# Kernel optimization log

Measured on AMD Instinct MI355X. Metric: run time of the kernel, lower is better.

## Reference

```python
import jax, jax.numpy as jnp
import numpy as np

# ---- config (matches init_kwargs) ----
B, S, V = 8, 900, 11
H, NH, HD = 512, 8, 64          # hidden, heads, head_dim = H // NH
L = 2                            # num_layers
EXPANSION = 4.0
INNER = 1536                     # find_multiple(round(4.0 * 512 * 2/3), 256)
STEPS = 2                        # mcmc_num_steps
EPS = 1e-5                       # rms_norm_eps
THETA = 10000.0                  # rope_theta
ESCALE = float(np.sqrt(H))       # embed_scale = sqrt(hidden_size)
SCALE = 1.0 / float(np.sqrt(HD))


def rms_norm(x):
    return x * jax.lax.rsqrt(jnp.mean(x * x, axis=-1, keepdims=True) + EPS)


def rope_tables():
    inv_freq = 1.0 / (THETA ** (jnp.arange(0, HD, 2, dtype=jnp.float32) / HD))
    t = jnp.arange(S, dtype=jnp.float32)
    freqs = jnp.outer(t, inv_freq)                # (S, HD/2)
    emb = jnp.concatenate([freqs, freqs], axis=-1)  # (S, HD)
    return jnp.cos(emb), jnp.sin(emb)


def rotate_half(x):
    x1, x2 = jnp.split(x, 2, axis=-1)
    return jnp.concatenate([-x2, x1], axis=-1)


def apply_rope(q, k, cos, sin):
    cos = cos[None, :, None, :]  # (1,S,1,HD) broadcast over batch & heads
    sin = sin[None, :, None, :]
    return q * cos + rotate_half(q) * sin, k * cos + rotate_half(k) * sin


def block(h, qkv_w, o_w, gu_w, d_w, cos, sin):
    b, s, _ = h.shape
    qkv = (h @ qkv_w).reshape(b, s, 3 * NH, HD)
    q, k, v = qkv[:, :, :NH], qkv[:, :, NH:2 * NH], qkv[:, :, 2 * NH:]
    q, k = apply_rope(q, k, cos, sin)
    scores = jnp.einsum('bqhd,bkhd->bhqk', q, k) * SCALE
    attn = jax.nn.softmax(scores, axis=-1)
    out = jnp.einsum('bhqk,bkhd->bqhd', attn, v).reshape(b, s, NH * HD)
    h = rms_norm(h + out @ o_w)                   # post-norm residual
    gu = h @ gu_w
    gate, up = gu[..., :INNER], gu[..., INNER:]
    h = rms_norm(h + (jax.nn.silu(gate) * up) @ d_w)
    return h


def energy(logits, embed_w, energy_w, qkv_w, o_w, gu_w, d_w, input_emb, cos, sin):
    probs = jax.nn.softmax(logits, axis=-1)       # soft token distribution
    h = input_emb + ESCALE * (probs @ embed_w)    # soft embedding
    for i in range(L):
        h = block(h, qkv_w[i], o_w[i], gu_w[i], d_w[i], cos, sin)
    return jnp.sum(h @ energy_w)                  # scalar energy


def setup_inputs() -> dict:
    key = jax.random.key(0)
    ks = jax.random.split(key, 8)
    inputs = jax.random.randint(ks[0], (B, S), 0, V, dtype=jnp.int64)
    puzzle_identifiers = jax.random.randint(ks[1], (B,), 0, 1, dtype=jnp.int64)
    init_std = 1.0 / ESCALE
    embed_w = jax.random.normal(ks[2], (V, H), jnp.float32) * init_std
    energy_w = jax.random.normal(ks[3], (H, 1), jnp.float32) * 0.02
    qkv_w = jax.random.normal(ks[4], (L, H, 3 * NH * HD), jnp.float32) * 0.02
    o_w = jax.random.normal(ks[5], (L, NH * HD, H), jnp.float32) * 0.02
    gu_w = jax.random.normal(ks[6], (L, H, 2 * INNER), jnp.float32) * 0.02
    d_w = jax.random.normal(ks[7], (L, INNER, H), jnp.float32) * 0.02
    alpha = jnp.asarray(100.0, jnp.float32)       # mcmc_step_size
    return {"inputs": inputs, "puzzle_identifiers": puzzle_identifiers,
            "embed_w": embed_w, "energy_w": energy_w, "qkv_w": qkv_w,
            "o_w": o_w, "gu_w": gu_w, "d_w": d_w, "alpha": alpha}


def reference(inputs, puzzle_identifiers, embed_w, energy_w, qkv_w, o_w, gu_w, d_w, alpha):
    cos, sin = rope_tables()
    input_emb = ESCALE * embed_w[inputs]          # (B,S,H)
    a = jnp.maximum(alpha, 1e-4)                  # torch.clamp(alpha, min=1e-4)
    logits = jnp.zeros((inputs.shape[0], S, V), jnp.float32)
    egrad = jax.grad(energy)
    for _ in range(STEPS):                        # MCMC energy-descent loop
        g = egrad(logits, embed_w, energy_w, qkv_w, o_w, gu_w, d_w, input_emb, cos, sin)
        logits = logits - a * g
    return logits
```

## Files before the change

### kernel.cpp

```cpp
#include <hip/hip_runtime.h>
#include <math.h>

#define B_ 8
#define S_ 900
#define V_ 11
#define H_ 512
#define NH_ 8
#define HD_ 64
#define INNER_ 1536
#define STEPS_ 2
#define NTOK (B_*S_)
#define EPS_ 1e-5f
#define THETA_ 10000.0f
#define ESCALE_ 22.627416997969522f
#define SCALE_ 0.125f
#define PT_ 68

typedef __attribute__((ext_vector_type(8))) short bh8;
typedef __attribute__((ext_vector_type(4))) float f32x4;
typedef __attribute__((ext_vector_type(4))) unsigned short us4;

union bfu { bh8 v; unsigned short s[8]; us4 q[2]; };

__device__ inline unsigned short f2bf(float x) {
  unsigned u = __builtin_bit_cast(unsigned, x);
  return (unsigned short)((u + 0x7FFFu + ((u >> 16) & 1u)) >> 16);
}
__device__ inline float b2f(unsigned short s) {
  return __builtin_bit_cast(float, (unsigned)s << 16);
}

__device__ inline void gld16(const unsigned short* g, unsigned short* l) {
  __builtin_amdgcn_global_load_lds(
      (const __attribute__((address_space(1))) void*)(g),
      (__attribute__((address_space(3))) void*)(l), 16, 0, 0);
}

__device__ inline bh8 lds16(const unsigned short* p) {
  bfu u;
  u.q[0] = *(const us4*)p;
  u.q[1] = *(const us4*)(p + 4);
  return u.v;
}
__device__ inline void sts16(unsigned short* p, bfu u) {
  *(us4*)p = u.q[0];
  *(us4*)(p + 4) = u.q[1];
}

__device__ inline float wave_sum64(float x) {
#pragma unroll
  for (int off = 32; off > 0; off >>= 1) x += __shfl_xor(x, off, 64);
  return x;
}

__device__ inline float quad_sum(float x) {
  x += __shfl_xor(x, 1, 64);
  x += __shfl_xor(x, 2, 64);
  return x;
}


__global__ void k_zero(float* p, int n) {
  int i = blockIdx.x * blockDim.x + threadIdx.x;
  if (i < n) p[i] = 0.f;
}

__global__ void k_rope_tables(float* cs, float* sn) {
  int idx = blockIdx.x * blockDim.x + threadIdx.x;
  if (idx >= S_ * 32) return;
  int s = idx >> 5, i = idx & 31;
  float freq = powf(THETA_, -(float)i / 32.0f);
  float ang = (float)s * freq;
  cs[idx] = cosf(ang);
  sn[idx] = sinf(ang);
}

__global__ void k_softmax_logits(const float* __restrict__ logits, float* __restrict__ P) {
  int t = blockIdx.x * blockDim.x + threadIdx.x;
  if (t >= NTOK) return;
  float x[V_];
  float m = -1e30f;
#pragma unroll
  for (int v = 0; v < V_; ++v) { x[v] = logits[t * V_ + v]; m = fmaxf(m, x[v]); }
  float ssum = 0.f;
#pragma unroll
  for (int v = 0; v < V_; ++v) { x[v] = expf(x[v] - m); ssum += x[v]; }
  float inv = 1.f / ssum;
#pragma unroll
  for (int v = 0; v < V_; ++v) P[t * V_ + v] = x[v] * inv;
}

__global__ void k_h0(const float* __restrict__ P, const float* __restrict__ E,
                     const int* __restrict__ inp, float* __restrict__ h0,
                     unsigned short* __restrict__ h016) {
  int t = blockIdx.x;
  int tid = threadIdx.x;
  __shared__ float p[V_];
  __shared__ int iw;
  if (tid < V_) p[tid] = P[t * V_ + tid];
  if (tid == 0) iw = inp[t];
  __syncthreads();
  for (int h = tid; h < H_; h += blockDim.x) {
    float acc = E[iw * H_ + h];
#pragma unroll
    for (int v = 0; v < V_; ++v) acc += p[v] * E[v * H_ + h];
    float val = ESCALE_ * acc;
    h0[(size_t)t * H_ + h] = val;
    h016[(size_t)t * H_ + h] = f2bf(val);
  }
}

__global__ void k_gfill(const float* __restrict__ ew, float* __restrict__ G) {
  int idx = blockIdx.x * blockDim.x + threadIdx.x;
  if (idx < NTOK * H_) G[idx] = ew[idx & (H_ - 1)];
}

__global__ void k_cast8(const float* __restrict__ X, unsigned short* __restrict__ Y, int n8) {
  int i = blockIdx.x * blockDim.x + threadIdx.x;
  if (i >= n8) return;
  const float4* p = (const float4*)(X + (size_t)i * 8);
  float4 a = p[0], b = p[1];
  bfu o;
  o.s[0] = f2bf(a.x); o.s[1] = f2bf(a.y); o.s[2] = f2bf(a.z); o.s[3] = f2bf(a.w);
  o.s[4] = f2bf(b.x); o.s[5] = f2bf(b.y); o.s[6] = f2bf(b.z); o.s[7] = f2bf(b.w);
  *(bh8*)(Y + (size_t)i * 8) = o.v;
}


__global__ void k_wt(const float* __restrict__ W, unsigned short* __restrict__ WT, int K, int N) {
  __shared__ float t[32][33];
  int k0 = blockIdx.y * 32, n0 = blockIdx.x * 32;
  int tx = threadIdx.x, ty = threadIdx.y;
#pragma unroll
  for (int i = 0; i < 4; ++i)
    t[ty + 8 * i][tx] = W[(size_t)(k0 + ty + 8 * i) * N + n0 + tx];
  __syncthreads();
#pragma unroll
  for (int i = 0; i < 4; ++i)
    WT[(size_t)(n0 + ty + 8 * i) * K + k0 + tx] = f2bf(t[tx][ty + 8 * i]);
}


template <int TM, int SILU_A, int ADD, int CBF, int ROPE, int SILUBWD>
__global__ __launch_bounds__(256) void k_gemm(const unsigned short* __restrict__ A16,
                                              const unsigned short* __restrict__ Bt,
                                              const float* __restrict__ Dm,
                                              float* __restrict__ Cf,
                                              unsigned short* __restrict__ C16,
                                              unsigned short* __restrict__ GU,
                                              const float* __restrict__ Cs,
                                              const float* __restrict__ Sn,
                                              int M, int N, int K, int lda) {
  __shared__ unsigned short As[TM][32];
  __shared__ unsigned short Bs[128][32];
  constexpr int FR = TM / 32;
  int tid = threadIdx.x;
  int m0 = blockIdx.y * TM, n0 = blockIdx.x * 128;
  int wid = tid >> 6, lane = tid & 63;
  int wr = (wid >> 1) * (FR * 16), wc = (wid & 1) * 64;
  int lr = lane & 15, lg = lane >> 4;
  int srow = lane >> 2, sck = (lane & 3) * 8;
  f32x4 acc[FR][4] = {};
  for (int k0 = 0; k0 < K; k0 += 32) {
    __syncthreads();
#pragma unroll
    for (int half = 0; half < TM / 64; ++half) {
      if (SILU_A) {
        int row = (tid >> 2) + 64 * half;
        int ck = (tid & 3) * 8;
        int gr = m0 + row; gr = gr < M ? gr : M - 1;
        const unsigned short* src = &A16[(size_t)gr * lda + k0 + ck];
        bfu pa;
#pragma unroll
        for (int j = 0; j < 8; ++j) {
          float g = b2f(src[j]), u = b2f(src[INNER_ + j]);
          pa.s[j] = f2bf((g / (1.f + __expf(-g))) * u);
        }
        *(bh8*)&As[row][ck] = pa.v;
      } else {
        int gr = m0 + 64 * half + wid * 16 + srow; gr = gr < M ? gr : M - 1;
        gld16(&A16[(size_t)gr * lda + k0 + sck], &As[64 * half + wid * 16][0]);
      }
    }
#pragma unroll
    for (int i = 0; i < 2; ++i) {
      int bb = wid * 2 + i;
      gld16(&Bt[(size_t)(n0 + bb * 16 + srow) * K + k0 + sck], &Bs[bb * 16][0]);
    }
    __syncthreads();
    bh8 av[FR], bv[4];
#pragma unroll
    for (int fr = 0; fr < FR; ++fr) av[fr] = *(const bh8*)&As[wr + fr * 16 + lr][lg * 8];
#pragma unroll
    for (int fc = 0; fc < 4; ++fc) bv[fc] = *(const bh8*)&Bs[wc + fc * 16 + lr][lg * 8];
#pragma unroll
    for (int fr = 0; fr < FR; ++fr)
#pragma unroll
      for (int fc = 0; fc < 4; ++fc)
        acc[fr][fc] = __builtin_amdgcn_mfma_f32_16x16x32_bf16(av[fr], bv[fc], acc[fr][fc], 0, 0, 0);
  }
  bool rope_on = ROPE && (((n0 + wc) >> 6) < 16);
#pragma unroll
  for (int fr = 0; fr < FR; ++fr) {
    int r0 = m0 + wr + fr * 16 + lg * 4;
#pragma unroll
    for (int i = 0; i < 4; ++i) {
      int gr = r0 + i;
      if (gr >= M) continue;
      float c0 = 1.f, s0 = 0.f, c1 = 1.f, s1 = 0.f;
      if (ROPE) {
        if (rope_on) {
          int s = gr % S_;
          c0 = Cs[s * 32 + lr];      s0 = Sn[s * 32 + lr];
          c1 = Cs[s * 32 + 16 + lr]; s1 = Sn[s * 32 + 16 + lr];
        }
      }
#pragma unroll
      for (int fc = 0; fc < 4; ++fc) {
        int gc = n0 + wc + fc * 16 + lr;
        float out = acc[fr][fc][i];
        if (ROPE) {
          float part = acc[fr][fc ^ 2][i];
          float cc = (fc & 1) ? c1 : c0;
          float ss = (fc & 1) ? s1 : s0;
          out = (fc < 2) ? (out * cc - part * ss) : (out * cc + part * ss);
        }
        if (ADD) out += Dm[(size_t)gr * N + gc];
        if (SILUBWD) {
          size_t gb = (size_t)gr * (size_t)(2 * INNER_) + gc;
          float g = b2f(GU[gb]), u = b2f(GU[gb + INNER_]);
          float sig = 1.f / (1.f + __expf(-g));
          GU[gb] = f2bf(out * u * sig * (1.f + g * (1.f - sig)));
          GU[gb + INNER_] = f2bf(out * g * sig);
        } else if (CBF) {
          C16[(size_t)gr * N + gc] = f2bf(out);
        } else {
          Cf[(size_t)gr * N + gc] = out;
        }
      }
    }
  }
}


__global__ __launch_bounds__(256) void k_attn_fwd3(const unsigned short* __restrict__ QKV,
                                                   unsigned short* __restrict__ AO,
                                                   float* __restrict__ MB,
                                                   float* __restrict__ LB) {
  __shared__ unsigned short Ks[64][PT_];
  __shared__ unsigned short VT[64][PT_];
  __shared__ unsigned short Ps[4][16][PT_];
  int tid = threadIdx.x;
  int h = blockIdx.y, b = blockIdx.z;
  int w = tid >> 6, lane = tid & 63;
  int lr = lane & 15, lg = lane >> 4;
  int q0 = blockIdx.x * 64 + w * 16;

  bh8 qf[2];
  {
    int qr = q0 + lr; if (qr >= S_) qr = S_ - 1;
    const unsigned short* qp = &QKV[((size_t)(b * S_ + qr) * 24 + h) * 64 + lg * 8];
    qf[0] = *(const bh8*)qp;
    qf[1] = *(const bh8*)(qp + 32);
  }
  f32x4 accO[4] = {};
  float m[4], lsum[4];
#pragma unroll
  for (int i = 0; i < 4; ++i) { m[i] = -1e30f; lsum[i] = 0.f; }

  for (int kt = 0; kt < S_; kt += 64) {
    __syncthreads();
    {
      int r = tid >> 2, c0 = (tid & 3) * 16;
      int src = kt + r;
      size_t ts = (size_t)b * S_ + (src < S_ ? src : S_ - 1);
      const unsigned short* gp = &QKV[(ts * 24 + 8 + h) * 64 + c0];
      bfu p0, p1;
      p0.v = *(const bh8*)gp;
      p1.v = *(const bh8*)(gp + 8);
      sts16(&Ks[r][c0], p0);
      sts16(&Ks[r][c0 + 8], p1);
    }
    {
      int d0 = (tid & 15) * 4, k0r = (tid >> 4) * 4;
      us4 rv[4];
#pragma unroll
      for (int j = 0; j < 4; ++j) {
        int src = kt + k0r + j;
        size_t ts = (size_t)b * S_ + (src < S_ ? src : S_ - 1);
        rv[j] = *(const us4*)&QKV[(ts * 24 + 16 + h) * 64 + d0];
      }
#pragma unroll
      for (int dd = 0; dd < 4; ++dd) {
        us4 pk = {rv[0][dd], rv[1][dd], rv[2][dd], rv[3][dd]};
        *(us4*)&VT[d0 + dd][k0r] = pk;
      }
    }
    __syncthreads();
    f32x4 accS[4] = {};
#pragma unroll
    for (int ks = 0; ks < 2; ++ks)
#pragma unroll
      for (int fk = 0; fk < 4; ++fk)
        accS[fk] = __builtin_amdgcn_mfma_f32_16x16x32_bf16(qf[ks], lds16(&Ks[fk * 16 + lr][ks * 32 + lg * 8]), accS[fk], 0, 0, 0);
    float sc[4][4], pmax[4];
#pragma unroll
    for (int i = 0; i < 4; ++i) pmax[i] = -1e30f;
#pragma unroll
    for (int fk = 0; fk < 4; ++fk)
#pragma unroll
      for (int i = 0; i < 4; ++i) {
        float s = accS[fk][i] * SCALE_;
        if (kt + fk * 16 + lr >= S_) s = -1e30f;
        sc[fk][i] = s;
        pmax[i] = fmaxf(pmax[i], s);
      }
#pragma unroll
    for (int i = 0; i < 4; ++i) {
      float v = pmax[i];
      v = fmaxf(v, __shfl_xor(v, 1, 64));
      v = fmaxf(v, __shfl_xor(v, 2, 64));
      v = fmaxf(v, __shfl_xor(v, 4, 64));
      v = fmaxf(v, __shfl_xor(v, 8, 64));
      pmax[i] = v;
    }
    float psum[4];
#pragma unroll
    for (int i = 0; i < 4; ++i) {
      float mn = fmaxf(m[i], pmax[i]);
      float eo = __expf(m[i] - mn);
      m[i] = mn;
      lsum[i] *= eo;
#pragma unroll
      for (int fd = 0; fd < 4; ++fd) accO[fd][i] *= eo;
      psum[i] = 0.f;
    }
#pragma unroll
    for (int fk = 0; fk < 4; ++fk)
#pragma unroll
      for (int i = 0; i < 4; ++i) {
        float p = __expf(sc[fk][i] - m[i]);
        sc[fk][i] = p;
        psum[i] += p;
      }
#pragma unroll
    for (int i = 0; i < 4; ++i) {
      float v = psum[i];
      v += __shfl_xor(v, 1, 64);
      v += __shfl_xor(v, 2, 64);
      v += __shfl_xor(v, 4, 64);
      v += __shfl_xor(v, 8, 64);
      lsum[i] += v;
    }
#pragma unroll
    for (int fk = 0; fk < 4; ++fk)
#pragma unroll
      for (int i = 0; i < 4; ++i)
        Ps[w][lg * 4 + i][fk * 16 + lr] = f2bf(sc[fk][i]);
#pragma unroll
    for (int ks = 0; ks < 2; ++ks) {
      bh8 ap = lds16(&Ps[w][lr][ks * 32 + lg * 8]);
#pragma unroll
      for (int fd = 0; fd < 4; ++fd)
        accO[fd] = __builtin_amdgcn_mfma_f32_16x16x32_bf16(ap, lds16(&VT[fd * 16 + lr][ks * 32 + lg * 8]), accO[fd], 0, 0, 0);
    }
  }
#pragma unroll
  for (int i = 0; i < 4; ++i) {
    int q = q0 + lg * 4 + i;
    if (q < S_) {
      float linv = 1.f / lsum[i];
      size_t obase = (size_t)(b * S_ + q) * H_ + h * 64;
#pragma unroll
      for (int fd = 0; fd < 4; ++fd) AO[obase + fd * 16 + lr] = f2bf(accO[fd][i] * linv);
      if (lr == 0) {
        MB[((size_t)b * NH_ + h) * S_ + q] = m[i];
        LB[((size_t)b * NH_ + h) * S_ + q] = linv;
      }
    }
  }
}

__global__ __launch_bounds__(256) void k_delta(const unsigned short* __restrict__ O,
                                               const unsigned short* __restrict__ dO,
                                               float* __restrict__ DB) {
  int tid = threadIdx.x;
  int h = blockIdx.y, b = blockIdx.z;
  int r = blockIdx.x * 64 + (tid >> 2), part = tid & 3;
  if (r >= S_) return;
  size_t base = (size_t)(b * S_ + r) * H_ + h * 64 + part * 16;
  bfu o0, o1, d0, d1;
  o0.v = *(const bh8*)&O[base];  o1.v = *(const bh8*)&O[base + 8];
  d0.v = *(const bh8*)&dO[base]; d1.v = *(const bh8*)&dO[base + 8];
  float s = 0.f;
#pragma unroll
  for (int j = 0; j < 8; ++j)
    s += b2f(o0.s[j]) * b2f(d0.s[j]) + b2f(o1.s[j]) * b2f(d1.s[j]);
  s = quad_sum(s);
  if (part == 0) DB[((size_t)b * NH_ + h) * S_ + r] = s;
}

__global__ __launch_bounds__(256) void k_attn_bwd_dq3(const unsigned short* __restrict__ QKV,
                                                      const unsigned short* __restrict__ dO,
                                                      const float* __restrict__ MB,
                                                      const float* __restrict__ LB,
                                                      const float* __restrict__ DB,
                                                      const float* __restrict__ Cs,
                                                      const float* __restrict__ Sn,
                                                      unsigned short* __restrict__ dQKV) {
  __shared__ unsigned short Ks[64][PT_];
  __shared__ unsigned short Vs[64][PT_];
  __shared__ unsigned short KT[64][PT_];
  __shared__ unsigned short Ps[4][16][PT_];
  int tid = threadIdx.x;
  int h = blockIdx.y, b = blockIdx.z;
  int w = tid >> 6, lane = tid & 63;
  int lr = lane & 15, lg = lane >> 4;
  int q0 = blockIdx.x * 64 + w * 16;
  size_t sbase = ((size_t)b * NH_ + h) * S_;

  bh8 qf[2], dof[2];
  {
    int qr = q0 + lr; if (qr >= S_) qr = S_ - 1;
    const unsigned short* qp = &QKV[((size_t)(b * S_ + qr) * 24 + h) * 64 + lg * 8];
    const unsigned short* dp = &dO[(size_t)(b * S_ + qr) * H_ + h * 64 + lg * 8];
    qf[0] = *(const bh8*)qp;  qf[1] = *(const bh8*)(qp + 32);
    dof[0] = *(const bh8*)dp; dof[1] = *(const bh8*)(dp + 32);
  }
  float mrow[4], lrow[4], drow[4];
#pragma unroll
  for (int i = 0; i < 4; ++i) {
    int q = q0 + lg * 4 + i; if (q >= S_) q = S_ - 1;
    mrow[i] = MB[sbase + q];
    lrow[i] = LB[sbase + q];
    drow[i] = DB[sbase + q];
  }
  f32x4 accQ[4] = {};

  for (int kt = 0; kt < S_; kt += 64) {
    __syncthreads();
    {
      int r = tid >> 2, c0 = (tid & 3) * 16;
      int src = kt + r;
      bool vld = src < S_;
      size_t ts = (size_t)b * S_ + (vld ? src : S_ - 1);
      const unsigned short* kp = &QKV[(ts * 24 + 8 + h) * 64 + c0];
      bfu p0{}, p1{}, p2{}, p3{};
      if (vld) {
        p0.v = *(const bh8*)kp;
        p1.v = *(const bh8*)(kp + 8);
        p2.v = *(const bh8*)(kp + 512);
        p3.v = *(const bh8*)(kp + 520);
      }
      sts16(&Ks[r][c0], p0); sts16(&Ks[r][c0 + 8], p1);
      sts16(&Vs[r][c0], p2); sts16(&Vs[r][c0 + 8], p3);
    }
    {
      int d0 = (tid & 15) * 4, k0r = (tid >> 4) * 4;
      us4 rv[4];
#pragma unroll
      for (int j = 0; j < 4; ++j) {
        int src = kt + k0r + j;
        bool vld = src < S_;
        size_t ts = (size_t)b * S_ + (vld ? src : S_ - 1);
        us4 t = *(const us4*)&QKV[(ts * 24 + 8 + h) * 64 + d0];
        if (!vld) t = us4{0, 0, 0, 0};
        rv[j] = t;
      }
#pragma unroll
      for (int dd = 0; dd < 4; ++dd) {
        us4 pk = {rv[0][dd], rv[1][dd], rv[2][dd], rv[3][dd]};
        *(us4*)&KT[d0 + dd][k0r] = pk;
      }
    }
    __syncthreads();
    f32x4 aS[4] = {}, aD[4] = {};
#pragma unroll
    for (int ks = 0; ks < 2; ++ks)
#pragma unroll
      for (int fk = 0; fk < 4; ++fk) {
        aS[fk] = __builtin_amdgcn_mfma_f32_16x16x32_bf16(qf[ks], lds16(&Ks[fk * 16 + lr][ks * 32 + lg * 8]), aS[fk], 0, 0, 0);
        aD[fk] = __builtin_amdgcn_mfma_f32_16x16x32_bf16(dof[ks], lds16(&Vs[fk * 16 + lr][ks * 32 + lg * 8]), aD[fk], 0, 0, 0);
      }
#pragma unroll
    for (int fk = 0; fk < 4; ++fk)
#pragma unroll
      for (int i = 0; i < 4; ++i) {
        float p = __expf(aS[fk][i] * SCALE_ - mrow[i]) * lrow[i];
        float ds = p * (aD[fk][i] - drow[i]);
        Ps[w][lg * 4 + i][fk * 16 + lr] = f2bf(ds);
      }
#pragma unroll
    for (int ks = 0; ks < 2; ++ks) {
      bh8 ap = lds16(&Ps[w][lr][ks * 32 + lg * 8]);
#pragma unroll
      for (int fd = 0; fd < 4; ++fd)
        accQ[fd] = __builtin_amdgcn_mfma_f32_16x16x32_bf16(ap, lds16(&KT[fd * 16 + lr][ks * 32 + lg * 8]), accQ[fd], 0, 0, 0);
    }
  }
#pragma unroll
  for (int i = 0; i < 4; ++i) {
    int q = q0 + lg * 4 + i;
    if (q < S_) {
      size_t obase = ((size_t)(b * S_ + q) * 24 + h) * 64;
      float c0 = Cs[q * 32 + lr], s0 = Sn[q * 32 + lr];
      float c1 = Cs[q * 32 + 16 + lr], s1 = Sn[q * 32 + 16 + lr];
#pragma unroll
      for (int fd = 0; fd < 4; ++fd) {
        float x = SCALE_ * accQ[fd][i];
        float p = SCALE_ * accQ[fd ^ 2][i];
        float cc = (fd & 1) ? c1 : c0;
        float ss = (fd & 1) ? s1 : s0;
        float out = (fd < 2) ? (x * cc + p * ss) : (x * cc - p * ss);
        dQKV[obase + fd * 16 + lr] = f2bf(out);
      }
    }
  }
}

__global__ __launch_bounds__(256) void k_attn_bwd_kv3(const unsigned short* __restrict__ QKV,
                                                      const unsigned short* __restrict__ dO,
                                                      const float* __restrict__ MB,
                                                      const float* __restrict__ LB,
                                                      const float* __restrict__ DB,
                                                      const float* __restrict__ Cs,
                                                      const float* __restrict__ Sn,
                                                      unsigned short* __restrict__ dQKV) {
  __shared__ unsigned short Qs[64][PT_];
  __shared__ unsigned short dOs[64][PT_];
  __shared__ unsigned short QT[64][PT_];
  __shared__ unsigned short dOT[64][PT_];
  __shared__ unsigned short Ps[4][16][PT_];
  __shared__ float sM[64], sL[64], sD[64];
  int tid = threadIdx.x;
  int h = blockIdx.y, b = blockIdx.z;
  int w = tid >> 6, lane = tid & 63;
  int lr = lane & 15, lg = lane >> 4;
  int k0w = blockIdx.x * 64 + w * 16;
  size_t sbase = ((size_t)b * NH_ + h) * S_;

  bh8 kf[2], vf[2];
  {
    int kr = k0w + lr; if (kr >= S_) kr = S_ - 1;
    const unsigned short* kp = &QKV[((size_t)(b * S_ + kr) * 24 + 8 + h) * 64 + lg * 8];
    kf[0] = *(const bh8*)kp;        kf[1] = *(const bh8*)(kp + 32);
    vf[0] = *(const bh8*)(kp + 512); vf[1] = *(const bh8*)(kp + 544);
  }
  f32x4 accK[4] = {}, accV[4] = {};

  for (int qt = 0; qt < S_; qt += 64) {
    __syncthreads();
    {
      int r = tid >> 2, c0 = (tid & 3) * 16;
      int src = qt + r;
      bool vld = src < S_;
      size_t ts = (size_t)b * S_ + (vld ? src : S_ - 1);
      const unsigned short* qp = &QKV[(ts * 24 + h) * 64 + c0];
      const unsigned short* dp = &dO[ts * H_ + h * 64 + c0];
      bfu p0, p1, p2{}, p3{};
      p0.v = *(const bh8*)qp;
      p1.v = *(const bh8*)(qp + 8);
      if (vld) {
        p2.v = *(const bh8*)dp;
        p3.v = *(const bh8*)(dp + 8);
      }
      sts16(&Qs[r][c0], p0);  sts16(&Qs[r][c0 + 8], p1);
      sts16(&dOs[r][c0], p2); sts16(&dOs[r][c0 + 8], p3);
    }
    {
      int d0 = (tid & 15) * 4, q0r = (tid >> 4) * 4;
      us4 rq[4], rd[4];
#pragma unroll
      for (int j = 0; j < 4; ++j) {
        int src = qt + q0r + j;
        bool vld = src < S_;
        size_t ts = (size_t)b * S_ + (vld ? src : S_ - 1);
        rq[j] = *(const us4*)&QKV[(ts * 24 + h) * 64 + d0];
        us4 td = *(const us4*)&dO[ts * H_ + h * 64 + d0];
        if (!vld) td = us4{0, 0, 0, 0};
        rd[j] = td;
      }
#pragma unroll
      for (int dd = 0; dd < 4; ++dd) {
        us4 pq = {rq[0][dd], rq[1][dd], rq[2][dd], rq[3][dd]};
        us4 pd = {rd[0][dd], rd[1][dd], rd[2][dd], rd[3][dd]};
        *(us4*)&QT[d0 + dd][q0r] = pq;
        *(us4*)&dOT[d0 + dd][q0r] = pd;
      }
    }
    if (tid < 64) {
      int src = qt + tid;
      bool vld = src < S_;
      int sc = vld ? src : S_ - 1;
      sM[tid] = MB[sbase + sc];
      sL[tid] = LB[sbase + sc];
      sD[tid] = vld ? DB[sbase + sc] : 0.f;
    }
    __syncthreads();
    f32x4 aS[4] = {}, aD[4] = {};
#pragma unroll
    for (int ks = 0; ks < 2; ++ks)
#pragma unroll
      for (int fq = 0; fq < 4; ++fq) {
        aS[fq] = __builtin_amdgcn_mfma_f32_16x16x32_bf16(kf[ks], lds16(&Qs[fq * 16 + lr][ks * 32 + lg * 8]), aS[fq], 0, 0, 0);
        aD[fq] = __builtin_amdgcn_mfma_f32_16x16x32_bf16(vf[ks], lds16(&dOs[fq * 16 + lr][ks * 32 + lg * 8]), aD[fq], 0, 0, 0);
      }
    float pv[4][4];
#pragma unroll
    for (int fq = 0; fq < 4; ++fq) {
      float mq = sM[fq * 16 + lr], lq = sL[fq * 16 + lr];
#pragma unroll
      for (int i = 0; i < 4; ++i) {
        float p = __expf(aS[fq][i] * SCALE_ - mq) * lq;
        pv[fq][i] = p;
        Ps[w][lg * 4 + i][fq * 16 + lr] = f2bf(p);
      }
    }
#pragma unroll
    for (int qs = 0; qs < 2; ++qs) {
      bh8 ap = lds16(&Ps[w][lr][qs * 32 + lg * 8]);
#pragma unroll
      for (int fd = 0; fd < 4; ++fd)
        accV[fd] = __builtin_amdgcn_mfma_f32_16x16x32_bf16(ap, lds16(&dOT[fd * 16 + lr][qs * 32 + lg * 8]), accV[fd], 0, 0, 0);
    }
#pragma unroll
    for (int fq = 0; fq < 4; ++fq) {
      float dq = sD[fq * 16 + lr];
#pragma unroll
      for (int i = 0; i < 4; ++i)
        Ps[w][lg * 4 + i][fq * 16 + lr] = f2bf(pv[fq][i] * (aD[fq][i] - dq));
    }
#pragma unroll
    for (int qs = 0; qs < 2; ++qs) {
      bh8 ap = lds16(&Ps[w][lr][qs * 32 + lg * 8]);
#pragma unroll
      for (int fd = 0; fd < 4; ++fd)
        accK[fd] = __builtin_amdgcn_mfma_f32_16x16x32_bf16(ap, lds16(&QT[fd * 16 + lr][qs * 32 + lg * 8]), accK[fd], 0, 0, 0);
    }
  }
#pragma unroll
  for (int i = 0; i < 4; ++i) {
    int k = k0w + lg * 4 + i;
    if (k < S_) {
      size_t obase = ((size_t)(b * S_ + k) * 24 + 8 + h) * 64;
      float c0 = Cs[k * 32 + lr], s0 = Sn[k * 32 + lr];
      float c1 = Cs[k * 32 + 16 + lr], s1 = Sn[k * 32 + 16 + lr];
#pragma unroll
      for (int fd = 0; fd < 4; ++fd) {
        float x = SCALE_ * accK[fd][i];
        float p = SCALE_ * accK[fd ^ 2][i];
        float cc = (fd & 1) ? c1 : c0;
        float ss = (fd & 1) ? s1 : s0;
        float out = (fd < 2) ? (x * cc + p * ss) : (x * cc - p * ss);
        dQKV[obase + fd * 16 + lr] = f2bf(out);
        dQKV[obase + 512 + fd * 16 + lr] = f2bf(accV[fd][i]);
      }
    }
  }
}


__global__ __launch_bounds__(256) void k_rms_fwd(const float* __restrict__ X, float* __restrict__ Y,
                                                 unsigned short* __restrict__ Y16) {
  int t = blockIdx.x, tid = threadIdx.x;
  float x0 = X[(size_t)t * H_ + tid], x1 = X[(size_t)t * H_ + tid + 256];
  __shared__ float red[256];
  red[tid] = x0 * x0 + x1 * x1;
  __syncthreads();
  for (int s = 128; s > 0; s >>= 1) {
    if (tid < s) red[tid] += red[tid + s];
    __syncthreads();
  }
  float r = rsqrtf(red[0] / H_ + EPS_);
  float y0 = x0 * r, y1 = x1 * r;
  Y[(size_t)t * H_ + tid] = y0;
  Y[(size_t)t * H_ + tid + 256] = y1;
  Y16[(size_t)t * H_ + tid] = f2bf(y0);
  Y16[(size_t)t * H_ + tid + 256] = f2bf(y1);
}

__global__ __launch_bounds__(256) void k_rms_bwd(const float* __restrict__ X,
                                                 const float* __restrict__ GY,
                                                 float* __restrict__ GX,
                                                 unsigned short* __restrict__ GX16) {
  int t = blockIdx.x, tid = threadIdx.x;
  float x0 = X[(size_t)t * H_ + tid], x1 = X[(size_t)t * H_ + tid + 256];
  float g0 = GY[(size_t)t * H_ + tid], g1 = GY[(size_t)t * H_ + tid + 256];
  __shared__ float r1[256], r2[256];
  r1[tid] = x0 * x0 + x1 * x1;
  r2[tid] = x0 * g0 + x1 * g1;
  __syncthreads();
  for (int s = 128; s > 0; s >>= 1) {
    if (tid < s) { r1[tid] += r1[tid + s]; r2[tid] += r2[tid + s]; }
    __syncthreads();
  }
  float r = rsqrtf(r1[0] / H_ + EPS_);
  float coef = r * r * r * r2[0] / (float)H_;
  float o0 = r * g0 - coef * x0, o1 = r * g1 - coef * x1;
  GX[(size_t)t * H_ + tid] = o0;
  GX[(size_t)t * H_ + tid + 256] = o1;
  GX16[(size_t)t * H_ + tid] = f2bf(o0);
  GX16[(size_t)t * H_ + tid + 256] = f2bf(o1);
}


__global__ __launch_bounds__(64) void k_logits_update(const float* __restrict__ G,
                                                      const float* __restrict__ E,
                                                      const float* __restrict__ P,
                                                      const float* __restrict__ alpha,
                                                      float* __restrict__ logits) {
  int t = blockIdx.x, lane = threadIdx.x;
  float dp[V_];
#pragma unroll
  for (int v = 0; v < V_; ++v) dp[v] = 0.f;
  for (int hh = lane; hh < H_; hh += 64) {
    float gh = G[(size_t)t * H_ + hh];
#pragma unroll
    for (int v = 0; v < V_; ++v) dp[v] += gh * E[v * H_ + hh];
  }
#pragma unroll
  for (int v = 0; v < V_; ++v) dp[v] = wave_sum64(dp[v]) * ESCALE_;
  float dot = 0.f;
  float pv[V_];
#pragma unroll
  for (int v = 0; v < V_; ++v) {
    pv[v] = P[t * V_ + v];
    dot += pv[v] * dp[v];
  }
  float a = fmaxf(alpha[0], 1e-4f);
  if (lane < V_) logits[t * V_ + lane] -= a * pv[lane] * (dp[lane] - dot);
}


struct Ctx {
  unsigned short *Q16, *Q016, *dQ16, *GU16, *DO16, *AO16, *AO016, *X116, *UDX16, *U016;
  float *X1, *X2, *X20, *G, *UDX, *P, *MB, *LB, *DB, *MB0, *LB0, *CS, *SN;
  const unsigned short *WTqkv[2], *WTo[2], *WTgu[2], *WTd[2];
  const unsigned short *WSqkv[2], *WSo[2], *WSgu[2], *WSd[2];
  hipStream_t st;
};

static void block_forward(Ctx& c, int l, const float* hin, const unsigned short* hin16,
                          float* hout, unsigned short* qb, unsigned short* ao,
                          float* mb, float* lb, float* x2buf, unsigned short* u16buf) {
  k_gemm<128, 0, 0, 1, 1, 0><<<dim3(3 * H_ / 128, (NTOK + 127) / 128), 256, 0, c.st>>>(
      hin16, c.WTqkv[l], nullptr, nullptr, qb, nullptr, c.CS, c.SN, NTOK, 3 * H_, H_, H_);
  k_attn_fwd3<<<dim3((S_ + 63) / 64, NH_, B_), 256, 0, c.st>>>(qb, ao, mb, lb);
  k_gemm<64, 0, 1, 0, 0, 0><<<dim3(H_ / 128, (NTOK + 63) / 64), 256, 0, c.st>>>(
      ao, c.WTo[l], hin, c.X1, nullptr, nullptr, nullptr, nullptr, NTOK, H_, H_, H_);
  k_rms_fwd<<<NTOK, 256, 0, c.st>>>(c.X1, c.UDX, u16buf);
  k_gemm<128, 0, 0, 1, 0, 0><<<dim3(2 * INNER_ / 128, (NTOK + 127) / 128), 256, 0, c.st>>>(
      u16buf, c.WTgu[l], nullptr, nullptr, c.GU16, nullptr, nullptr, nullptr, NTOK, 2 * INNER_, H_, H_);
  k_gemm<64, 1, 1, 0, 0, 0><<<dim3(H_ / 128, (NTOK + 63) / 64), 256, 0, c.st>>>(
      c.GU16, c.WTd[l], c.UDX, x2buf, nullptr, nullptr, nullptr, nullptr, NTOK, H_, INNER_, 2 * INNER_);
  if (hout) k_rms_fwd<<<NTOK, 256, 0, c.st>>>(x2buf, hout, c.UDX16);
}

static void block_backward(Ctx& c, int l, const float* hin, const unsigned short* hin16,
                           unsigned short* qb, unsigned short* ao, float* mb, float* lb,
                           bool full) {
  const float* x2src;
  if (full) {
    block_forward(c, l, hin, hin16, nullptr, qb, ao, mb, lb, c.X2, c.UDX16);
    x2src = c.X2;
  } else {
    k_gemm<64, 0, 1, 0, 0, 0><<<dim3(H_ / 128, (NTOK + 63) / 64), 256, 0, c.st>>>(
        ao, c.WTo[l], hin, c.X1, nullptr, nullptr, nullptr, nullptr, NTOK, H_, H_, H_);
    k_gemm<128, 0, 0, 1, 0, 0><<<dim3(2 * INNER_ / 128, (NTOK + 127) / 128), 256, 0, c.st>>>(
        c.U016, c.WTgu[l], nullptr, nullptr, c.GU16, nullptr, nullptr, nullptr, NTOK, 2 * INNER_, H_, H_);
    x2src = c.X20;
  }
  k_rms_bwd<<<NTOK, 256, 0, c.st>>>(x2src, c.G, c.UDX, c.UDX16);
  k_gemm<128, 0, 0, 0, 0, 1><<<dim3(INNER_ / 128, (NTOK + 127) / 128), 256, 0, c.st>>>(
      c.UDX16, c.WSd[l], nullptr, nullptr, nullptr, c.GU16, nullptr, nullptr, NTOK, INNER_, H_, H_);
  k_gemm<64, 0, 1, 0, 0, 0><<<dim3(H_ / 128, (NTOK + 63) / 64), 256, 0, c.st>>>(
      c.GU16, c.WSgu[l], c.UDX, c.G, nullptr, nullptr, nullptr, nullptr, NTOK, H_, 2 * INNER_, 2 * INNER_);
  k_rms_bwd<<<NTOK, 256, 0, c.st>>>(c.X1, c.G, c.UDX, c.UDX16);
  k_gemm<64, 0, 0, 1, 0, 0><<<dim3(H_ / 128, (NTOK + 63) / 64), 256, 0, c.st>>>(
      c.UDX16, c.WSo[l], nullptr, nullptr, c.DO16, nullptr, nullptr, nullptr, NTOK, H_, H_, H_);
  dim3 agrid((S_ + 63) / 64, NH_, B_);
  k_delta<<<agrid, 256, 0, c.st>>>(ao, c.DO16, c.DB);
  k_attn_bwd_dq3<<<agrid, 256, 0, c.st>>>(qb, c.DO16, mb, lb, c.DB, c.CS, c.SN, c.dQ16);
  k_attn_bwd_kv3<<<agrid, 256, 0, c.st>>>(qb, c.DO16, mb, lb, c.DB, c.CS, c.SN, c.dQ16);
  k_gemm<64, 0, 1, 0, 0, 0><<<dim3(H_ / 128, (NTOK + 63) / 64), 256, 0, c.st>>>(
      c.dQ16, c.WSqkv[l], c.UDX, c.G, nullptr, nullptr, nullptr, nullptr, NTOK, H_, 3 * H_, 3 * H_);
}

extern "C" void kernel_launch(void* const* d_in, const int* in_sizes, int n_in,
                              void* d_out, int out_size, void* d_ws, size_t ws_size,
                              hipStream_t stream) {
  const int* inputs = (const int*)d_in[0];
  const float* E = (const float*)d_in[2];
  const float* ew = (const float*)d_in[3];
  const float* qkvw = (const float*)d_in[4];
  const float* ow = (const float*)d_in[5];
  const float* guw = (const float*)d_in[6];
  const float* dw = (const float*)d_in[7];
  const float* alpha = (const float*)d_in[8];
  float* logits = (float*)d_out;

  const size_t WT_FLOATS = 3407872;
  const size_t NEED =
      3 * ((size_t)NTOK * 3 * H_ / 2) +
      ((size_t)NTOK * INNER_) +
      5 * ((size_t)NTOK * H_) +
      6 * ((size_t)NTOK * H_ / 2) +
      ((size_t)NTOK * V_) +
      5 * ((size_t)B_ * NH_ * S_) +
      2 * ((size_t)S_ * 32) +
      2 * WT_FLOATS;
  if (ws_size < NEED * sizeof(float)) {
    k_zero<<<(NTOK * V_ + 255) / 256, 256, 0, stream>>>(logits, NTOK * V_);
    return;
  }

  float* f = (float*)d_ws;
  Ctx c;
  c.st = stream;
  c.Q16 = (unsigned short*)f;  f += (size_t)NTOK * 3 * H_ / 2;
  c.Q016 = (unsigned short*)f; f += (size_t)NTOK * 3 * H_ / 2;
  c.dQ16 = (unsigned short*)f; f += (size_t)NTOK * 3 * H_ / 2;
  c.GU16 = (unsigned short*)f; f += (size_t)NTOK * INNER_;
  c.X1 = f;   f += (size_t)NTOK * H_;
  c.X2 = f;   f += (size_t)NTOK * H_;
  c.X20 = f;  f += (size_t)NTOK * H_;
  c.G = f;    f += (size_t)NTOK * H_;
  c.UDX = f;  f += (size_t)NTOK * H_;
  c.AO16 = (unsigned short*)f;  f += (size_t)NTOK * H_ / 2;
  c.AO016 = (unsigned short*)f; f += (size_t)NTOK * H_ / 2;
  c.DO16 = (unsigned short*)f;  f += (size_t)NTOK * H_ / 2;
  c.X116 = (unsigned short*)f;  f += (size_t)NTOK * H_ / 2;
  c.UDX16 = (unsigned short*)f; f += (size_t)NTOK * H_ / 2;
  c.U016 = (unsigned short*)f;  f += (size_t)NTOK * H_ / 2;
  c.P = f;    f += (size_t)NTOK * V_;
  c.MB = f;   f += (size_t)B_ * NH_ * S_;
  c.LB = f;   f += (size_t)B_ * NH_ * S_;
  c.DB = f;   f += (size_t)B_ * NH_ * S_;
  c.MB0 = f;  f += (size_t)B_ * NH_ * S_;
  c.LB0 = f;  f += (size_t)B_ * NH_ * S_;
  c.CS = f;   f += (size_t)S_ * 32;
  c.SN = f;   f += (size_t)S_ * 32;
  unsigned short* wt = (unsigned short*)f;

  const size_t LQKV = (size_t)H_ * 3 * H_;
  const size_t LO = (size_t)H_ * H_;
  const size_t LGU = (size_t)H_ * 2 * INNER_;
  const size_t LD = (size_t)INNER_ * H_;

  for (int l = 0; l < 2; ++l) {
    c.WTqkv[l] = wt;
    k_wt<<<dim3(3 * H_ / 32, H_ / 32), dim3(32, 8), 0, stream>>>(qkvw + l * LQKV, wt, H_, 3 * H_);
    wt += LQKV;
    c.WTo[l] = wt;
    k_wt<<<dim3(H_ / 32, H_ / 32), dim3(32, 8), 0, stream>>>(ow + l * LO, wt, H_, H_);
    wt += LO;
    c.WTgu[l] = wt;
    k_wt<<<dim3(2 * INNER_ / 32, H_ / 32), dim3(32, 8), 0, stream>>>(guw + l * LGU, wt, H_, 2 * INNER_);
    wt += LGU;
    c.WTd[l] = wt;
    k_wt<<<dim3(H_ / 32, INNER_ / 32), dim3(32, 8), 0, stream>>>(dw + l * LD, wt, INNER_, H_);
    wt += LD;
  }
  {
    unsigned short* ws = wt;
    k_cast8<<<(int)((2 * LQKV / 8 + 255) / 256), 256, 0, stream>>>(qkvw, ws, (int)(2 * LQKV / 8));
    c.WSqkv[0] = ws; c.WSqkv[1] = ws + LQKV; ws += 2 * LQKV;
    k_cast8<<<(int)((2 * LO / 8 + 255) / 256), 256, 0, stream>>>(ow, ws, (int)(2 * LO / 8));
    c.WSo[0] = ws; c.WSo[1] = ws + LO; ws += 2 * LO;
    k_cast8<<<(int)((2 * LGU / 8 + 255) / 256), 256, 0, stream>>>(guw, ws, (int)(2 * LGU / 8));
    c.WSgu[0] = ws; c.WSgu[1] = ws + LGU; ws += 2 * LGU;
    k_cast8<<<(int)((2 * LD / 8 + 255) / 256), 256, 0, stream>>>(dw, ws, (int)(2 * LD / 8));
    c.WSd[0] = ws; c.WSd[1] = ws + LD;
  }

  k_zero<<<(NTOK * V_ + 255) / 256, 256, 0, stream>>>(logits, NTOK * V_);
  k_rope_tables<<<(S_ * 32 + 255) / 256, 256, 0, stream>>>(c.CS, c.SN);

  for (int step = 0; step < STEPS_; ++step) {
    k_softmax_logits<<<(NTOK + 255) / 256, 256, 0, stream>>>(logits, c.P);
    k_h0<<<NTOK, 256, 0, stream>>>(c.P, E, inputs, c.X1, c.X116);
    block_forward(c, 0, c.X1, c.X116, c.UDX, c.Q016, c.AO016, c.MB0, c.LB0, c.X20, c.U016);
    k_gfill<<<(NTOK * H_ + 255) / 256, 256, 0, stream>>>(ew, c.G);
    block_backward(c, 1, c.UDX, c.UDX16, c.Q16, c.AO16, c.MB, c.LB, true);
    k_h0<<<NTOK, 256, 0, stream>>>(c.P, E, inputs, c.X1, c.X116);
    block_backward(c, 0, c.X1, c.X116, c.Q016, c.AO016, c.MB0, c.LB0, false);
    k_logits_update<<<NTOK, 64, 0, stream>>>(c.G, E, c.P, alpha, logits);
  }
}
```

Measured before the change: 2.430 ms.

## Prefetch next K/V/Q/dO tiles into registers in attention kernels

In the forward attention kernel and both backward kernels (dQ and dK/dV), the global loads for the next 64-row tile are now issued into registers right after the current tile is written to shared memory. This lets global-memory latency overlap the MFMA and softmax work of the current iteration, at the cost of more live registers per thread. The shared-memory row padding also changes from 68 to 70 elements to alter the bank mapping. A 140-byte row stride breaks 16-byte and 8-byte alignment of the vector LDS reads and writes, which risks split or slower LDS accesses.

```diff
diff --git a/kernel.cpp b/kernel.cpp
--- a/kernel.cpp
+++ b/kernel.cpp
@@ -14,7 +14,7 @@
 #define THETA_ 10000.0f
 #define ESCALE_ 22.627416997969522f
 #define SCALE_ 0.125f
-#define PT_ 68
+#define PT_ 70
 
 typedef __attribute__((ext_vector_type(8))) short bh8;
 typedef __attribute__((ext_vector_type(4))) float f32x4;
@@ -255,6 +255,8 @@
   int w = tid >> 6, lane = tid & 63;
   int lr = lane & 15, lg = lane >> 4;
   int q0 = blockIdx.x * 64 + w * 16;
+  int sr = tid >> 2, sc0 = (tid & 3) * 16;
+  int vd0 = (tid & 15) * 4, vk0 = (tid >> 4) * 4;
 
   bh8 qf[2];
   {
@@ -268,32 +270,42 @@
 #pragma unroll
   for (int i = 0; i < 4; ++i) { m[i] = -1e30f; lsum[i] = 0.f; }
 
+  bfu kA, kB;
+  us4 vR[4];
+  {
+    int src = sr;
+    size_t ts = (size_t)b * S_ + (src < S_ ? src : S_ - 1);
+    const unsigned short* gp = &QKV[(ts * 24 + 8 + h) * 64 + sc0];
+    kA.v = *(const bh8*)gp;
+    kB.v = *(const bh8*)(gp + 8);
+#pragma unroll
+    for (int j = 0; j < 4; ++j) {
+      int s2 = vk0 + j;
+      size_t t2 = (size_t)b * S_ + (s2 < S_ ? s2 : S_ - 1);
+      vR[j] = *(const us4*)&QKV[(t2 * 24 + 16 + h) * 64 + vd0];
+    }
+  }
+
   for (int kt = 0; kt < S_; kt += 64) {
     __syncthreads();
-    {
-      int r = tid >> 2, c0 = (tid & 3) * 16;
-      int src = kt + r;
+    sts16(&Ks[sr][sc0], kA);
+    sts16(&Ks[sr][sc0 + 8], kB);
+#pragma unroll
+    for (int dd = 0; dd < 4; ++dd) {
+      us4 pk = {vR[0][dd], vR[1][dd], vR[2][dd], vR[3][dd]};
+      *(us4*)&VT[vd0 + dd][vk0] = pk;
+    }
+    if (kt + 64 < S_) {
+      int src = kt + 64 + sr;
       size_t ts = (size_t)b * S_ + (src < S_ ? src : S_ - 1);
-      const unsigned short* gp = &QKV[(ts * 24 + 8 + h) * 64 + c0];
-      bfu p0, p1;
-      p0.v = *(const bh8*)gp;
-      p1.v = *(const bh8*)(gp + 8);
-      sts16(&Ks[r][c0], p0);
-      sts16(&Ks[r][c0 + 8], p1);
-    }
-    {
-      int d0 = (tid & 15) * 4, k0r = (tid >> 4) * 4;
-      us4 rv[4];
+      const unsigned short* gp = &QKV[(ts * 24 + 8 + h) * 64 + sc0];
+      kA.v = *(const bh8*)gp;
+      kB.v = *(const bh8*)(gp + 8);
 #pragma unroll
       for (int j = 0; j < 4; ++j) {
-        int src = kt + k0r + j;
-        size_t ts = (size_t)b * S_ + (src < S_ ? src : S_ - 1);
-        rv[j] = *(const us4*)&QKV[(ts * 24 + 16 + h) * 64 + d0];
-      }
-#pragma unroll
-      for (int dd = 0; dd < 4; ++dd) {
-        us4 pk = {rv[0][dd], rv[1][dd], rv[2][dd], rv[3][dd]};
-        *(us4*)&VT[d0 + dd][k0r] = pk;
+        int s2 = kt + 64 + vk0 + j;
+        size_t t2 = (size_t)b * S_ + (s2 < S_ ? s2 : S_ - 1);
+        vR[j] = *(const us4*)&QKV[(t2 * 24 + 16 + h) * 64 + vd0];
       }
     }
     __syncthreads();
@@ -418,6 +430,8 @@
   int lr = lane & 15, lg = lane >> 4;
   int q0 = blockIdx.x * 64 + w * 16;
   size_t sbase = ((size_t)b * NH_ + h) * S_;
+  int sr = tid >> 2, sc0 = (tid & 3) * 16;
+  int vd0 = (tid & 15) * 4, vk0 = (tid >> 4) * 4;
 
   bh8 qf[2], dof[2];
   {
@@ -437,40 +451,59 @@
   }
   f32x4 accQ[4] = {};
 
+  bfu pA{}, pB{}, pC{}, pD{};
+  us4 rv[4];
+  {
+    int src = sr;
+    bool vld = src < S_;
+    size_t ts = (size_t)b * S_ + (vld ? src : S_ - 1);
+    const unsigned short* kp = &QKV[(ts * 24 + 8 + h) * 64 + sc0];
+    if (vld) {
+      pA.v = *(const bh8*)kp;
+      pB.v = *(const bh8*)(kp + 8);
+      pC.v = *(const bh8*)(kp + 512);
+      pD.v = *(const bh8*)(kp + 520);
+    }
+#pragma unroll
+    for (int j = 0; j < 4; ++j) {
+      int s2 = vk0 + j;
+      bool v2 = s2 < S_;
+      size_t t2 = (size_t)b * S_ + (v2 ? s2 : S_ - 1);
+      us4 t = *(const us4*)&QKV[(t2 * 24 + 8 + h) * 64 + vd0];
+      if (!v2) t = us4{0, 0, 0, 0};
+      rv[j] = t;
+    }
+  }
+
   for (int kt = 0; kt < S_; kt += 64) {
     __syncthreads();
-    {
-      int r = tid >> 2, c0 = (tid & 3) * 16;
-      int src = kt + r;
+    sts16(&Ks[sr][sc0], pA); sts16(&Ks[sr][sc0 + 8], pB);
+    sts16(&Vs[sr][sc0], pC); sts16(&Vs[sr][sc0 + 8], pD);
+#pragma unroll
+    for (int dd = 0; dd < 4; ++dd) {
+      us4 pk = {rv[0][dd], rv[1][dd], rv[2][dd], rv[3][dd]};
+      *(us4*)&KT[vd0 + dd][vk0] = pk;
+    }
+    if (kt + 64 < S_) {
+      int src = kt + 64 + sr;
       bool vld = src < S_;
       size_t ts = (size_t)b * S_ + (vld ? src : S_ - 1);
-      const unsigned short* kp = &QKV[(ts * 24 + 8 + h) * 64 + c0];
-      bfu p0{}, p1{}, p2{}, p3{};
+      const unsigned short* kp = &QKV[(ts * 24 + 8 + h) * 64 + sc0];
+      pA = bfu{}; pB = bfu{}; pC = bfu{}; pD = bfu{};
       if (vld) {
-        p0.v = *(const bh8*)kp;
-        p1.v = *(const bh8*)(kp + 8);
-        p2.v = *(const bh8*)(kp + 512);
-        p3.v = *(const bh8*)(kp + 520);
-      }
-      sts16(&Ks[r][c0], p0); sts16(&Ks[r][c0 + 8], p1);
-      sts16(&Vs[r][c0], p2); sts16(&Vs[r][c0 + 8], p3);
-    }
-    {
-      int d0 = (tid & 15) * 4, k0r = (tid >> 4) * 4;
-      us4 rv[4];
+        pA.v = *(const bh8*)kp;
+        pB.v = *(const bh8*)(kp + 8);
+        pC.v = *(const bh8*)(kp + 512);
+        pD.v = *(const bh8*)(kp + 520);
+      }
 #pragma unroll
       for (int j = 0; j < 4; ++j) {
-        int src = kt + k0r + j;
-        bool vld = src < S_;
-        size_t ts = (size_t)b * S_ + (vld ? src : S_ - 1);
-        us4 t = *(const us4*)&QKV[(ts * 24 + 8 + h) * 64 + d0];
-        if (!vld) t = us4{0, 0, 0, 0};
+        int s2 = kt + 64 + vk0 + j;
+        bool v2 = s2 < S_;
+        size_t t2 = (size_t)b * S_ + (v2 ? s2 : S_ - 1);
+        us4 t = *(const us4*)&QKV[(t2 * 24 + 8 + h) * 64 + vd0];
+        if (!v2) t = us4{0, 0, 0, 0};
         rv[j] = t;
-      }
-#pragma unroll
-      for (int dd = 0; dd < 4; ++dd) {
-        us4 pk = {rv[0][dd], rv[1][dd], rv[2][dd], rv[3][dd]};
-        *(us4*)&KT[d0 + dd][k0r] = pk;
       }
     }
     __syncthreads();
@@ -538,6 +571,8 @@
   int lr = lane & 15, lg = lane >> 4;
   int k0w = blockIdx.x * 64 + w * 16;
   size_t sbase = ((size_t)b * NH_ + h) * S_;
+  int sr = tid >> 2, sc0 = (tid & 3) * 16;
+  int vd0 = (tid & 15) * 4, vk0 = (tid >> 4) * 4;
 
   bh8 kf[2], vf[2];
   {
@@ -548,53 +583,87 @@
   }
   f32x4 accK[4] = {}, accV[4] = {};
 
+  bfu pA, pB, pC{}, pD{};
+  us4 rq[4], rd[4];
+  float stM = 0.f, stL = 0.f, stD = 0.f;
+  {
+    int src = sr;
+    bool vld = src < S_;
+    size_t ts = (size_t)b * S_ + (vld ? src : S_ - 1);
+    const unsigned short* qp = &QKV[(ts * 24 + h) * 64 + sc0];
+    const unsigned short* dp = &dO[ts * H_ + h * 64 + sc0];
+    pA.v = *(const bh8*)qp;
+    pB.v = *(const bh8*)(qp + 8);
+    if (vld) {
+      pC.v = *(const bh8*)dp;
+      pD.v = *(const bh8*)(dp + 8);
+    }
+#pragma unroll
+    for (int j = 0; j < 4; ++j) {
+      int s2 = vk0 + j;
+      bool v2 = s2 < S_;
+      size_t t2 = (size_t)b * S_ + (v2 ? s2 : S_ - 1);
+      rq[j] = *(const us4*)&QKV[(t2 * 24 + h) * 64 + vd0];
+      us4 td = *(const us4*)&dO[t2 * H_ + h * 64 + vd0];
+      if (!v2) td = us4{0, 0, 0, 0};
+      rd[j] = td;
+    }
+    if (tid < 64) {
+      bool v2 = tid < S_;
+      int sc = v2 ? tid : S_ - 1;
+      stM = MB[sbase + sc];
+      stL = LB[sbase + sc];
+      stD = v2 ? DB[sbase + sc] : 0.f;
+    }
+  }
+
   for (int qt = 0; qt < S_; qt += 64) {
     __syncthreads();
-    {
-      int r = tid >> 2, c0 = (tid & 3) * 16;
-      int src = qt + r;
+    sts16(&Qs[sr][sc0], pA);  sts16(&Qs[sr][sc0 + 8], pB);
+    sts16(&dOs[sr][sc0], pC); sts16(&dOs[sr][sc0 + 8], pD);
+#pragma unroll
+    for (int dd = 0; dd < 4; ++dd) {
+      us4 pq = {rq[0][dd], rq[1][dd], rq[2][dd], rq[3][dd]};
+      us4 pd = {rd[0][dd], rd[1][dd], rd[2][dd], rd[3][dd]};
+      *(us4*)&QT[vd0 + dd][vk0] = pq;
+      *(us4*)&dOT[vd0 + dd][vk0] = pd;
+    }
+    if (tid < 64) {
+      sM[tid] = stM;
+      sL[tid] = stL;
+      sD[tid] = stD;
+    }
+    if (qt + 64 < S_) {
+      int src = qt + 64 + sr;
       bool vld = src < S_;
       size_t ts = (size_t)b * S_ + (vld ? src : S_ - 1);
-      const unsigned short* qp = &QKV[(ts * 24 + h) * 64 + c0];
-      const unsigned short* dp = &dO[ts * H_ + h * 64 + c0];
-      bfu p0, p1, p2{}, p3{};
-      p0.v = *(const bh8*)qp;
-      p1.v = *(const bh8*)(qp + 8);
+      const unsigned short* qp = &QKV[(ts * 24 + h) * 64 + sc0];
+      const unsigned short* dp = &dO[ts * H_ + h * 64 + sc0];
+      pA.v = *(const bh8*)qp;
+      pB.v = *(const bh8*)(qp + 8);
+      pC = bfu{}; pD = bfu{};
       if (vld) {
-        p2.v = *(const bh8*)dp;
-        p3.v = *(const bh8*)(dp + 8);
-      }
-      sts16(&Qs[r][c0], p0);  sts16(&Qs[r][c0 + 8], p1);
-      sts16(&dOs[r][c0], p2); sts16(&dOs[r][c0 + 8], p3);
-    }
-    {
-      int d0 = (tid & 15) * 4, q0r = (tid >> 4) * 4;
-      us4 rq[4], rd[4];
+        pC.v = *(const bh8*)dp;
+        pD.v = *(const bh8*)(dp + 8);
+      }
 #pragma unroll
       for (int j = 0; j < 4; ++j) {
-        int src = qt + q0r + j;
-        bool vld = src < S_;
-        size_t ts = (size_t)b * S_ + (vld ? src : S_ - 1);
-        rq[j] = *(const us4*)&QKV[(ts * 24 + h) * 64 + d0];
-        us4 td = *(const us4*)&dO[ts * H_ + h * 64 + d0];
-        if (!vld) td = us4{0, 0, 0, 0};
+        int s2 = qt + 64 + vk0 + j;
+        bool v2 = s2 < S_;
+        size_t t2 = (size_t)b * S_ + (v2 ? s2 : S_ - 1);
+        rq[j] = *(const us4*)&QKV[(t2 * 24 + h) * 64 + vd0];
+        us4 td = *(const us4*)&dO[t2 * H_ + h * 64 + vd0];
+        if (!v2) td = us4{0, 0, 0, 0};
         rd[j] = td;
       }
-#pragma unroll
-      for (int dd = 0; dd < 4; ++dd) {
-        us4 pq = {rq[0][dd], rq[1][dd], rq[2][dd], rq[3][dd]};
-        us4 pd = {rd[0][dd], rd[1][dd], rd[2][dd], rd[3][dd]};
-        *(us4*)&QT[d0 + dd][q0r] = pq;
-        *(us4*)&dOT[d0 + dd][q0r] = pd;
-      }
-    }
-    if (tid < 64) {
-      int src = qt + tid;
-      bool vld = src < S_;
-      int sc = vld ? src : S_ - 1;
-      sM[tid] = MB[sbase + sc];
-      sL[tid] = LB[sbase + sc];
-      sD[tid] = vld ? DB[sbase + sc] : 0.f;
+      if (tid < 64) {
+        int s2 = qt + 64 + tid;
+        bool v2 = s2 < S_;
+        int sc = v2 ? s2 : S_ - 1;
+        stM = MB[sbase + sc];
+        stL = LB[sbase + sc];
+        stD = v2 ? DB[sbase + sc] : 0.f;
+      }
     }
     __syncthreads();
     f32x4 aS[4] = {}, aD[4] = {};
```

Measured after the change: 6.534 ms. +168.9%, slower.
